# Kernel optimization log

Hardware: AMD Instinct MI355X
Metric: run time of the kernel (lower is better)

The kernel has to match this reference:

```python
import jax, jax.numpy as jnp
import numpy as np

D = 256        # d_model
E = 1024       # num_experts (== 4*d_model, required by the broadcast in forward)
F = 4 * D      # expert output width (== E)
N = 4096       # tokens; must be >= E since forward indexes weights[0..E-1]


def setup_inputs() -> dict:
    key = jax.random.key(0)
    k_x, k_gw, k_ew, k_eb = jax.random.split(key, 4)
    x = jax.random.normal(k_x, (N, D), dtype=jnp.float32)
    gate_W = jax.random.normal(k_gw, (D, E), dtype=jnp.float32) * 0.02
    gate_b = jnp.zeros((E,), dtype=jnp.float32)
    expert_W = jax.random.normal(k_ew, (E, D, F), dtype=jnp.float32) * 0.02
    expert_b = jax.random.normal(k_eb, (E, F), dtype=jnp.float32) * 0.02
    return {"x": x, "gate_W": gate_W, "gate_b": gate_b,
            "expert_W": expert_W, "expert_b": expert_b}


def reference(x, gate_W, gate_b, expert_W, expert_b):
    # weights: [N, E] softmax over experts
    weights = jax.nn.softmax(x @ gate_W + gate_b, axis=-1)
    # Original: out = sum_i weights[i] * (x @ W_i + b_i)
    # weights[i] is ROW i (token i) of the gate softmax, shape [E] == [F],
    # broadcast over tokens. Collapse the sum over experts into an effective
    # weight matrix instead of materializing [E, N, F]:
    w = weights[:E]                               # [E, F] rows 0..E-1
    W_eff = jnp.einsum('ef,edf->df', w, expert_W)  # [D, F]
    b_eff = jnp.einsum('ef,ef->f', w, expert_b)    # [F]
    return x @ W_eff + b_eff                       # [N, F]
```

## Files before the change

### kernel.cpp

```cpp
#include <hip/hip_runtime.h>
#include <math.h>


#define DD 256
#define EE 1024
#define FF 1024
#define NN 4096

__global__ __launch_bounds__(256) void gate_kernel(const float* __restrict__ x,
                                                   const float* __restrict__ gW,
                                                   const float* __restrict__ gb,
                                                   float* __restrict__ w_out) {
    __shared__ float xs[4 * DD];
    __shared__ float ls[4 * EE];
    const int tid = threadIdx.x;
    const int r0 = blockIdx.x * 4;

    ((float4*)xs)[tid] = ((const float4*)(x + (size_t)r0 * DD))[tid];
    __syncthreads();

    float4 a0 = {0,0,0,0}, a1 = {0,0,0,0}, a2 = {0,0,0,0}, a3 = {0,0,0,0};
    const float4* gw4 = (const float4*)gW;
    #pragma unroll 4
    for (int d = 0; d < DD; ++d) {
        float4 g = gw4[d * 256 + tid];
        float x0 = xs[0*DD + d], x1 = xs[1*DD + d], x2 = xs[2*DD + d], x3 = xs[3*DD + d];
        a0.x += x0*g.x; a0.y += x0*g.y; a0.z += x0*g.z; a0.w += x0*g.w;
        a1.x += x1*g.x; a1.y += x1*g.y; a1.z += x1*g.z; a1.w += x1*g.w;
        a2.x += x2*g.x; a2.y += x2*g.y; a2.z += x2*g.z; a2.w += x2*g.w;
        a3.x += x3*g.x; a3.y += x3*g.y; a3.z += x3*g.z; a3.w += x3*g.w;
    }
    float4 b = ((const float4*)gb)[tid];
    a0.x += b.x; a0.y += b.y; a0.z += b.z; a0.w += b.w;
    a1.x += b.x; a1.y += b.y; a1.z += b.z; a1.w += b.w;
    a2.x += b.x; a2.y += b.y; a2.z += b.z; a2.w += b.w;
    a3.x += b.x; a3.y += b.y; a3.z += b.z; a3.w += b.w;
    ((float4*)&ls[0*EE])[tid] = a0;
    ((float4*)&ls[1*EE])[tid] = a1;
    ((float4*)&ls[2*EE])[tid] = a2;
    ((float4*)&ls[3*EE])[tid] = a3;
    __syncthreads();

    const int lane = tid & 63;
    const int row = tid >> 6;
    float vals[16];
    float m = -3.0e38f;
    #pragma unroll
    for (int i = 0; i < 16; ++i) {
        vals[i] = ls[row * EE + i * 64 + lane];
        m = fmaxf(m, vals[i]);
    }
    #pragma unroll
    for (int off = 1; off < 64; off <<= 1) m = fmaxf(m, __shfl_xor(m, off));
    float s = 0.0f;
    #pragma unroll
    for (int i = 0; i < 16; ++i) {
        vals[i] = __expf(vals[i] - m);
        s += vals[i];
    }
    #pragma unroll
    for (int off = 1; off < 64; off <<= 1) s += __shfl_xor(s, off);
    const float inv = 1.0f / s;
    float* wrow = w_out + (size_t)(r0 + row) * EE;
    #pragma unroll
    for (int i = 0; i < 16; ++i) wrow[i * 64 + lane] = vals[i] * inv;
}

__global__ __launch_bounds__(256) void weff_kernel(const float* __restrict__ eW,
                                                   const float* __restrict__ eb,
                                                   const float* __restrict__ w,
                                                   float* __restrict__ weff) {
    const int tid = threadIdx.x;
    const int slice = blockIdx.x >> 2;
    const int chunk = blockIdx.x & 3;
    const int f = tid * 4;

    const float* p;
    size_t estride;
    if (slice < DD) {
        p = eW + (size_t)slice * FF + f;
        estride = (size_t)DD * FF;
    } else {
        p = eb + f;
        estride = FF;
    }
    const int e0 = chunk * 256;
    p += (size_t)e0 * estride;
    const float* q = w + (size_t)e0 * EE + f;

    float4 acc = {0,0,0,0};
    #pragma unroll 4
    for (int i = 0; i < 256; ++i) {
        float4 a = *(const float4*)p;
        float4 ww = *(const float4*)q;
        acc.x += a.x * ww.x;
        acc.y += a.y * ww.y;
        acc.z += a.z * ww.z;
        acc.w += a.w * ww.w;
        p += estride;
        q += EE;
    }
    float* dst = weff + (size_t)slice * FF + f;
    atomicAdd(dst + 0, acc.x);
    atomicAdd(dst + 1, acc.y);
    atomicAdd(dst + 2, acc.z);
    atomicAdd(dst + 3, acc.w);
}

__global__ __launch_bounds__(256) void out_kernel(const float* __restrict__ x,
                                                  const float* __restrict__ weff,
                                                  float* __restrict__ out) {
    __shared__ float xs[16 * DD];
    const int tid = threadIdx.x;
    const int n0 = blockIdx.x * 16;

    {
        const float4* xsrc = (const float4*)(x + (size_t)n0 * DD);
        float4* xd = (float4*)xs;
        #pragma unroll
        for (int k = 0; k < 4; ++k) xd[tid + k * 256] = xsrc[tid + k * 256];
    }
    __syncthreads();

    float4 acc[16];
    #pragma unroll
    for (int r = 0; r < 16; ++r) acc[r] = make_float4(0.f, 0.f, 0.f, 0.f);

    const float4* wp = (const float4*)weff + tid;
    #pragma unroll 2
    for (int d = 0; d < DD; ++d) {
        float4 g = wp[d * 256];
        #pragma unroll
        for (int r = 0; r < 16; ++r) {
            float xv = xs[r * DD + d];
            acc[r].x += xv * g.x;
            acc[r].y += xv * g.y;
            acc[r].z += xv * g.z;
            acc[r].w += xv * g.w;
        }
    }

    float4 b = ((const float4*)(weff + (size_t)DD * FF))[tid];
    #pragma unroll
    for (int r = 0; r < 16; ++r) {
        float4 o;
        o.x = acc[r].x + b.x;
        o.y = acc[r].y + b.y;
        o.z = acc[r].z + b.z;
        o.w = acc[r].w + b.w;
        ((float4*)(out + (size_t)(n0 + r) * FF))[tid] = o;
    }
}

extern "C" void kernel_launch(void* const* d_in, const int* in_sizes, int n_in,
                              void* d_out, int out_size, void* d_ws, size_t ws_size,
                              hipStream_t stream) {
    const float* x  = (const float*)d_in[0];
    const float* gW = (const float*)d_in[1];
    const float* gb = (const float*)d_in[2];
    const float* eW = (const float*)d_in[3];
    const float* eb = (const float*)d_in[4];
    float* out = (float*)d_out;

    float* ws   = (float*)d_ws;
    float* w    = ws;
    float* weff = ws + (size_t)EE * EE;

    hipMemsetAsync(weff, 0, (size_t)(DD + 1) * FF * sizeof(float), stream);

    gate_kernel<<<dim3(256), dim3(256), 0, stream>>>(x, gW, gb, w);
    weff_kernel<<<dim3(1028), dim3(256), 0, stream>>>(eW, eb, w, weff);
    out_kernel<<<dim3(256), dim3(256), 0, stream>>>(x, weff, out);
}
```

Baseline: 1.460 ms.

## Retile W_eff reduction to reuse gate weights across eight d-rows

The expert-weight reduction is reorganized so each block handles 8 consecutive d rows over a 64-expert chunk. Each loaded gate-weight vector is reused across eight expert-weight rows, and the bias reduction moves to 16 dedicated blocks. Expert weights are read with nontemporal loads so the 1 GB stream does not pollute cache. The output GEMM halves its rows per block to 8 to double the grid size, and uses nontemporal stores. The trade-off is more atomic adds and higher register use per thread in the reduction kernel.

```diff
diff --git a/kernel.cpp b/kernel.cpp
--- a/kernel.cpp
+++ b/kernel.cpp
@@ -6,6 +6,8 @@
 #define EE 1024
 #define FF 1024
 #define NN 4096
+
+typedef float f32x4 __attribute__((ext_vector_type(4)));
 
 __global__ __launch_bounds__(256) void gate_kernel(const float* __restrict__ x,
                                                    const float* __restrict__ gW,
@@ -71,84 +73,102 @@
                                                    const float* __restrict__ w,
                                                    float* __restrict__ weff) {
     const int tid = threadIdx.x;
-    const int slice = blockIdx.x >> 2;
-    const int chunk = blockIdx.x & 3;
     const int f = tid * 4;
+    const int b = blockIdx.x;
 
-    const float* p;
-    size_t estride;
-    if (slice < DD) {
-        p = eW + (size_t)slice * FF + f;
-        estride = (size_t)DD * FF;
-    } else {
-        p = eb + f;
-        estride = FF;
+    if (b < 16) {
+        const int e0 = b * 64;
+        const float* pw = w  + (size_t)e0 * EE + f;
+        const float* pb = eb + (size_t)e0 * FF + f;
+        f32x4 acc = {0.f, 0.f, 0.f, 0.f};
+        #pragma unroll 4
+        for (int i = 0; i < 64; ++i) {
+            f32x4 wv = *(const f32x4*)pw;
+            f32x4 a  = __builtin_nontemporal_load((const f32x4*)pb);
+            acc += wv * a;
+            pw += EE;
+            pb += FF;
+        }
+        float* dst = weff + (size_t)DD * FF + f;
+        atomicAdd(dst + 0, acc.x);
+        atomicAdd(dst + 1, acc.y);
+        atomicAdd(dst + 2, acc.z);
+        atomicAdd(dst + 3, acc.w);
+        return;
     }
-    const int e0 = chunk * 256;
-    p += (size_t)e0 * estride;
-    const float* q = w + (size_t)e0 * EE + f;
 
-    float4 acc = {0,0,0,0};
-    #pragma unroll 4
-    for (int i = 0; i < 256; ++i) {
-        float4 a = *(const float4*)p;
-        float4 ww = *(const float4*)q;
-        acc.x += a.x * ww.x;
-        acc.y += a.y * ww.y;
-        acc.z += a.z * ww.z;
-        acc.w += a.w * ww.w;
-        p += estride;
-        q += EE;
+    const int m = b - 16;
+    const int dgroup = m >> 4;
+    const int echunk = m & 15;
+    const int e0 = echunk * 64;
+    const int d0 = dgroup * 8;
+
+    const float* pw = w  + (size_t)e0 * EE + f;
+    const float* pe = eW + (size_t)e0 * DD * FF + (size_t)d0 * FF + f;
+
+    f32x4 acc[8];
+    #pragma unroll
+    for (int k = 0; k < 8; ++k) acc[k] = (f32x4){0.f, 0.f, 0.f, 0.f};
+
+    #pragma unroll 2
+    for (int i = 0; i < 64; ++i) {
+        f32x4 wv = *(const f32x4*)pw;
+        f32x4 a[8];
+        #pragma unroll
+        for (int k = 0; k < 8; ++k)
+            a[k] = __builtin_nontemporal_load((const f32x4*)(pe + (size_t)k * FF));
+        #pragma unroll
+        for (int k = 0; k < 8; ++k)
+            acc[k] += wv * a[k];
+        pw += EE;
+        pe += (size_t)DD * FF;
     }
-    float* dst = weff + (size_t)slice * FF + f;
-    atomicAdd(dst + 0, acc.x);
-    atomicAdd(dst + 1, acc.y);
-    atomicAdd(dst + 2, acc.z);
-    atomicAdd(dst + 3, acc.w);
+
+    #pragma unroll
+    for (int k = 0; k < 8; ++k) {
+        float* dst = weff + (size_t)(d0 + k) * FF + f;
+        atomicAdd(dst + 0, acc[k].x);
+        atomicAdd(dst + 1, acc[k].y);
+        atomicAdd(dst + 2, acc[k].z);
+        atomicAdd(dst + 3, acc[k].w);
+    }
 }
 
 __global__ __launch_bounds__(256) void out_kernel(const float* __restrict__ x,
                                                   const float* __restrict__ weff,
                                                   float* __restrict__ out) {
-    __shared__ float xs[16 * DD];
+    __shared__ float xs[8 * DD];
     const int tid = threadIdx.x;
-    const int n0 = blockIdx.x * 16;
+    const int n0 = blockIdx.x * 8;
 
     {
-        const float4* xsrc = (const float4*)(x + (size_t)n0 * DD);
-        float4* xd = (float4*)xs;
+        const f32x4* xsrc = (const f32x4*)(x + (size_t)n0 * DD);
+        f32x4* xd = (f32x4*)xs;
         #pragma unroll
-        for (int k = 0; k < 4; ++k) xd[tid + k * 256] = xsrc[tid + k * 256];
+        for (int k = 0; k < 2; ++k) xd[tid + k * 256] = xsrc[tid + k * 256];
     }
     __syncthreads();
 
-    float4 acc[16];
+    f32x4 acc[8];
     #pragma unroll
-    for (int r = 0; r < 16; ++r) acc[r] = make_float4(0.f, 0.f, 0.f, 0.f);
+    for (int r = 0; r < 8; ++r) acc[r] = (f32x4){0.f, 0.f, 0.f, 0.f};
 
-    const float4* wp = (const float4*)weff + tid;
-    #pragma unroll 2
+    const f32x4* wp = (const f32x4*)weff + tid;
+    #pragma unroll 4
     for (int d = 0; d < DD; ++d) {
-        float4 g = wp[d * 256];
+        f32x4 g = wp[(size_t)d * 256];
         #pragma unroll
-        for (int r = 0; r < 16; ++r) {
+        for (int r = 0; r < 8; ++r) {
             float xv = xs[r * DD + d];
-            acc[r].x += xv * g.x;
-            acc[r].y += xv * g.y;
-            acc[r].z += xv * g.z;
-            acc[r].w += xv * g.w;
+            acc[r] += g * xv;
         }
     }
 
-    float4 b = ((const float4*)(weff + (size_t)DD * FF))[tid];
+    f32x4 bv = ((const f32x4*)(weff + (size_t)DD * FF))[tid];
     #pragma unroll
-    for (int r = 0; r < 16; ++r) {
-        float4 o;
-        o.x = acc[r].x + b.x;
-        o.y = acc[r].y + b.y;
-        o.z = acc[r].z + b.z;
-        o.w = acc[r].w + b.w;
-        ((float4*)(out + (size_t)(n0 + r) * FF))[tid] = o;
+    for (int r = 0; r < 8; ++r) {
+        f32x4 o = acc[r] + bv;
+        __builtin_nontemporal_store(o, (f32x4*)(out + (size_t)(n0 + r) * FF) + tid);
     }
 }
 
@@ -169,6 +189,6 @@
     hipMemsetAsync(weff, 0, (size_t)(DD + 1) * FF * sizeof(float), stream);
 
     gate_kernel<<<dim3(256), dim3(256), 0, stream>>>(x, gW, gb, w);
-    weff_kernel<<<dim3(1028), dim3(256), 0, stream>>>(eW, eb, w, weff);
-    out_kernel<<<dim3(256), dim3(256), 0, stream>>>(x, weff, out);
+    weff_kernel<<<dim3(528), dim3(256), 0, stream>>>(eW, eb, w, weff);
+    out_kernel<<<dim3(512), dim3(256), 0, stream>>>(x, weff, out);
 }
```

Result: no change. 1.439 ms (-1.4%).
